# Kernel optimization log

Hardware: AMD Instinct MI355X
Metric: run time of the kernel (lower is better)

## Reference

```python
import jax, jax.numpy as jnp
import numpy as np

EMB = 768
BLOCK = 64
K = EMB // BLOCK  # 12


def setup_inputs() -> dict:
    key = jax.random.key(0)
    ks = jax.random.split(key, 8)
    n, c, d, h, E, M, P = 4, 1024, 768, 12, 32, 4, 256
    seq = jax.random.normal(ks[0], (n, c, d), dtype=jnp.float32)
    attn = jax.random.uniform(ks[1], (n, h, c, c), dtype=jnp.float32)
    attn = attn / attn.sum(-1, keepdims=True)  # attention-like rows
    mention_pos = jax.random.randint(ks[2], (n, E, M), 0, c)
    hts = jax.random.randint(ks[3], (n, P, 2), 0, E)
    W_head = jax.random.normal(ks[4], (2 * d, EMB), dtype=jnp.float32) / np.sqrt(2 * d)
    W_tail = jax.random.normal(ks[5], (2 * d, EMB), dtype=jnp.float32) / np.sqrt(2 * d)
    W_bil = jax.random.normal(ks[6], (EMB * BLOCK, 97), dtype=jnp.float32) / np.sqrt(EMB * BLOCK)
    return {
        "sequence_output": seq,
        "attention": attn,
        "mention_pos": mention_pos,
        "hts": hts,
        "W_head": W_head,
        "b_head": jnp.zeros((EMB,), jnp.float32),
        "W_tail": W_tail,
        "b_tail": jnp.zeros((EMB,), jnp.float32),
        "W_bil": W_bil,
        "b_bil": jnp.zeros((97,), jnp.float32),
    }


def reference(sequence_output, attention, mention_pos, hts,
              W_head, b_head, W_tail, b_tail, W_bil, b_bil):
    n, c, d = sequence_output.shape
    h = attention.shape[1]
    P = hts.shape[1]

    bidx = jnp.arange(n)[:, None, None]
    # gather mention token embeddings: [n, E, M, d]
    m_emb = sequence_output[bidx, mention_pos]
    # entity embedding = logsumexp over mentions (single-mention case is identical)
    ent_emb = jax.nn.logsumexp(m_emb, axis=2)                      # [n, E, d]

    # per-mention attention rows: attention[i, :, pos, :] -> [n, E, M, h, c]
    att_t = jnp.transpose(attention, (0, 2, 1, 3))                 # [n, c, h, c]
    m_att = att_t[bidx, mention_pos]                               # [n, E, M, h, c]
    ent_att = m_att.mean(axis=2)                                   # [n, E, h, c]

    pidx = jnp.arange(n)[:, None]
    hs = ent_emb[pidx, hts[..., 0]]                                # [n, P, d]
    ts = ent_emb[pidx, hts[..., 1]]
    h_att = ent_att[pidx, hts[..., 0]]                             # [n, P, h, c]
    t_att = ent_att[pidx, hts[..., 1]]

    ht_att = (h_att * t_att).mean(axis=2)                          # [n, P, c]
    ht_att = ht_att / (ht_att.sum(-1, keepdims=True) + 1e-30)
    # relation context: contract('ld,rl->rd') per doc
    rs = jnp.einsum('ncd,npc->npd', sequence_output, ht_att)       # [n, P, d]

    R = n * P
    hs2 = jnp.tanh(jnp.concatenate([hs, rs], -1).reshape(R, 2 * d) @ W_head + b_head)
    ts2 = jnp.tanh(jnp.concatenate([ts, rs], -1).reshape(R, 2 * d) @ W_tail + b_tail)

    b1 = hs2.reshape(R, K, BLOCK)
    b2 = ts2.reshape(R, K, BLOCK)
    bl = (b1[:, :, :, None] * b2[:, :, None, :]).reshape(R, EMB * BLOCK)
    logits = bl @ W_bil + b_bil                                    # [R, 97]
    return logits
```

## Files before the change

### kernel.cpp

```cpp
#include <hip/hip_runtime.h>
#include <hip/hip_bf16.h>
#include <math.h>

#define ND 4
#define CL 1024
#define DD 768
#define HH 12
#define EE 32
#define MMEN 4
#define PP 256
#define EMBD 768
#define KBL 12
#define OUTD 97
#define RTOT (ND*PP)
#define NSPLIT 24

typedef unsigned short u16;
typedef __attribute__((ext_vector_type(8))) short short8;
typedef __attribute__((ext_vector_type(8))) _Float16 half8;
typedef __attribute__((ext_vector_type(4))) float f32x4;

static __device__ inline float bf16u_to_f(unsigned v){
  union { unsigned u; float f; } c; c.u = v << 16; return c.f;
}
static __device__ inline unsigned f_to_bf16u(float f){
  union { float f; unsigned u; } c; c.f = f;
  return (c.u + 0x7fffu + ((c.u >> 16) & 1u)) >> 16;
}
static __device__ inline u16 f_to_f16u(float f){
  _Float16 h = (_Float16)f;
  union { _Float16 h; u16 u; } c; c.h = h; return c.u;
}

#define GLOAD_LDS16(gp, lp) __builtin_amdgcn_global_load_lds( \
    (const __attribute__((address_space(1))) unsigned*)(gp), \
    (__attribute__((address_space(3))) unsigned*)(lp), 16, 0, 0)

__global__ __launch_bounds__(256) void k_preproc(
    const float* __restrict__ seq, const float* __restrict__ attn,
    const int* __restrict__ mpos,
    const float* __restrict__ W_head, const float* __restrict__ W_tail,
    const float* __restrict__ W_bil,
    u16* __restrict__ ent_emb_bf, u16* __restrict__ ent_att_bf,
    u16* __restrict__ seq_t_bf, u16* __restrict__ Wh_t, u16* __restrict__ Wt_t,
    u16* __restrict__ Wt2, float* __restrict__ S)
{
  __shared__ float t[32][33];
  __shared__ __align__(16) u16 lds2[4480];
  const int bid = blockIdx.x;
  const int tid = threadIdx.x;

  if (bid < 384) {
    int idx = bid*256 + tid;
    if (idx < RTOT) S[idx] = 0.f;
    int dd = idx % DD;
    int e  = (idx / DD) % EE;
    int i  = idx / (DD*EE);
    const int* mp = mpos + (i*EE + e)*MMEN;
    float v[MMEN];
    float mx = -1e30f;
    #pragma unroll
    for (int m=0;m<MMEN;m++){
      v[m] = seq[(i*CL + mp[m])*DD + dd];
      mx = fmaxf(mx, v[m]);
    }
    float s = 0.f;
    #pragma unroll
    for (int m=0;m<MMEN;m++) s += expf(v[m]-mx);
    ent_emb_bf[idx] = (u16)f_to_bf16u(mx + logf(s));
  }
  else if (bid < 1152) {
    int idx = (bid-384)*256 + tid;
    int j8   = idx % (CL/8);
    int head = (idx / (CL/8)) % HH;
    int e    = (idx / (CL/8*HH)) % EE;
    int i    = idx / (CL/8*HH*EE);
    const int* mp = mpos + (i*EE + e)*MMEN;
    float acc[8] = {};
    #pragma unroll
    for (int m=0;m<MMEN;m++){
      const float4* p = (const float4*)(attn +
          ((size_t)(i*HH + head)*CL + mp[m])*CL + j8*8);
      float4 a = p[0], b = p[1];
      acc[0]+=a.x; acc[1]+=a.y; acc[2]+=a.z; acc[3]+=a.w;
      acc[4]+=b.x; acc[5]+=b.y; acc[6]+=b.z; acc[7]+=b.w;
    }
    unsigned o[4];
    #pragma unroll
    for (int q=0;q<4;q++){
      unsigned lo = f_to_bf16u(acc[2*q]   * (1.f/MMEN));
      unsigned hi = f_to_bf16u(acc[2*q+1] * (1.f/MMEN));
      o[q] = lo | (hi<<16);
    }
    ((uint4*)ent_att_bf)[idx] = make_uint4(o[0],o[1],o[2],o[3]);
  }
  else if (bid < 4224) {
    int l = bid - 1152;
    int bx = l % 24;
    int by = (l / 24) % 32;
    int bz = l / 768;
    const int R = CL, C = DD;
    const float* src = seq + (size_t)bz*R*C;
    u16* dst = seq_t_bf + (size_t)bz*R*C;
    int tx = tid & 31, ty = tid >> 5;
    int c0 = bx*32, r0 = by*32;
    #pragma unroll
    for (int q=0;q<4;q++)
      t[ty+8*q][tx] = src[(size_t)(r0+ty+8*q)*C + c0+tx];
    __syncthreads();
    #pragma unroll
    for (int q=0;q<4;q++)
      dst[(size_t)(c0+ty+8*q)*R + r0+tx] = (u16)f_to_bf16u(t[tx][ty+8*q]);
  }
  else if (bid < 6528) {
    int l = bid - 4224;
    int bx = l % 24;
    int by = (l / 24) % 48;
    int bz = l / 1152;
    const int R = 1536, C = DD;
    const float* src = bz ? W_tail : W_head;
    u16* dst         = bz ? Wt_t   : Wh_t;
    int tx = tid & 31, ty = tid >> 5;
    int c0 = bx*32, r0 = by*32;
    #pragma unroll
    for (int q=0;q<4;q++)
      t[ty+8*q][tx] = src[(size_t)(r0+ty+8*q)*C + c0+tx];
    __syncthreads();
    #pragma unroll
    for (int q=0;q<4;q++)
      dst[(size_t)(c0+ty+8*q)*R + r0+tx] = (u16)f_to_bf16u(t[tx][ty+8*q]);
  }
  else {
    int cc = bid - 6528;
    for (int u=tid; u<4480; u+=256) lds2[u] = 0;
    __syncthreads();
    for (int u=tid; u<112*32; u+=256){
      int kk = u / 112, n = u % 112;
      if (n < OUTD)
        lds2[n*40 + kk] = f_to_f16u(W_bil[(size_t)(cc*32 + kk)*OUTD + n]);
    }
    __syncthreads();
    uint4* dst = (uint4*)(Wt2 + (size_t)cc*4480);
    const uint4* src = (const uint4*)lds2;
    for (int v=tid; v<560; v+=256) dst[v] = src[v];
  }
}

__global__ __launch_bounds__(256) void k_ht_att(const u16* __restrict__ ent_att_bf,
    const int* __restrict__ hts, u16* __restrict__ u_ht_bf, float* __restrict__ S)
{
  const int j0  = blockIdx.x*64;
  const int pb  = blockIdx.y*64;
  const int doc = blockIdx.z;
  const int tid = threadIdx.x;
  const int p_local = tid >> 2, quad = tid & 3;
  const int grow = doc*PP + pb + p_local;
  const int he = hts[grow*2+0], te = hts[grow*2+1];
  const u16* ha = ent_att_bf + ((size_t)(doc*EE + he)*HH)*CL;
  const u16* ta = ent_att_bf + ((size_t)(doc*EE + te)*HH)*CL;
  const int jj = j0 + quad*16;

  float acc[16] = {};
  #pragma unroll
  for (int h=0; h<HH; h++){
    const uint4* pa = (const uint4*)(ha + h*CL + jj);
    const uint4* pb4 = (const uint4*)(ta + h*CL + jj);
    uint4 a0 = pa[0], a1 = pa[1];
    uint4 b0 = pb4[0], b1 = pb4[1];
    unsigned ua[8] = {a0.x,a0.y,a0.z,a0.w,a1.x,a1.y,a1.z,a1.w};
    unsigned ub[8] = {b0.x,b0.y,b0.z,b0.w,b1.x,b1.y,b1.z,b1.w};
    #pragma unroll
    for (int q=0;q<8;q++){
      acc[2*q]   += bf16u_to_f(ua[q]&0xffffu) * bf16u_to_f(ub[q]&0xffffu);
      acc[2*q+1] += bf16u_to_f(ua[q]>>16)     * bf16u_to_f(ub[q]>>16);
    }
  }
  float sum = 0.f;
  unsigned o[8];
  #pragma unroll
  for (int q=0;q<8;q++){
    float v0 = acc[2*q]   * (1.f/HH);
    float v1 = acc[2*q+1] * (1.f/HH);
    sum += v0 + v1;
    o[q] = f_to_bf16u(v0) | (f_to_bf16u(v1)<<16);
  }
  uint4* dst = (uint4*)(u_ht_bf + (size_t)grow*CL + jj);
  dst[0] = make_uint4(o[0],o[1],o[2],o[3]);
  dst[1] = make_uint4(o[4],o[5],o[6],o[7]);
  sum += __shfl_xor(sum, 1, 64);
  sum += __shfl_xor(sum, 2, 64);
  if (quad == 0) atomicAdd(&S[grow], sum);
}

__global__ __launch_bounds__(256) void k_gemm_rs_mfma(
    const u16* __restrict__ u_ht_bf, const u16* __restrict__ seq_t_bf,
    const float* __restrict__ S, u16* __restrict__ rs_bf)
{
  const int rt = blockIdx.x, ct = blockIdx.y, doc = blockIdx.z;
  const u16* A  = u_ht_bf + (size_t)doc*PP*CL;
  const u16* Bt = seq_t_bf + (size_t)doc*DD*CL;
  const int row0 = rt*64, col0 = ct*64;
  __shared__ __align__(16) u16 As[64*64];
  __shared__ __align__(16) u16 Bs[64*64];
  const int tid = threadIdx.x, lane = tid & 63, wave = tid >> 6;
  const int m = lane & 15, j8 = lane >> 4;
  const int srow8 = lane >> 3, sc8 = lane & 7;
  f32x4 acc[4];
  #pragma unroll
  for (int b=0;b<4;b++) acc[b] = (f32x4){0.f,0.f,0.f,0.f};

  for (int k0 = 0; k0 < CL; k0 += 64){
    __syncthreads();
    #pragma unroll
    for (int ii=0; ii<2; ii++){
      int row = ii*32 + wave*8 + srow8;
      int gc = sc8 ^ (row & 7);
      const u16* gpA = A + (size_t)(row0+row)*CL + k0 + gc*8;
      GLOAD_LDS16(gpA, &As[(ii*32 + wave*8)*64]);
      const u16* gpB = Bt + (size_t)(col0+row)*CL + k0 + gc*8;
      GLOAD_LDS16(gpB, &Bs[(ii*32 + wave*8)*64]);
    }
    __syncthreads();
    #pragma unroll
    for (int h=0; h<2; h++){
      short8 af, bf[4];
      {
        int r = wave*16 + m;
        int c = (h*4 + j8) ^ (r & 7);
        af = *(const short8*)&As[r*64 + c*8];
      }
      #pragma unroll
      for (int nt=0; nt<4; nt++){
        int n = nt*16 + m;
        int c = (h*4 + j8) ^ (n & 7);
        bf[nt] = *(const short8*)&Bs[n*64 + c*8];
      }
      #pragma unroll
      for (int nt=0; nt<4; nt++)
        acc[nt] = __builtin_amdgcn_mfma_f32_16x16x32_bf16(af, bf[nt], acc[nt], 0,0,0);
    }
  }

  float sc[4];
  #pragma unroll
  for (int reg=0; reg<4; reg++){
    int rowg = doc*PP + row0 + wave*16 + j8*4 + reg;
    sc[reg] = 1.f / (S[rowg] + 1e-30f);
  }
  #pragma unroll
  for (int nt=0; nt<4; nt++){
    int colg = col0 + nt*16 + m;
    #pragma unroll
    for (int reg=0; reg<4; reg++){
      int rowg = doc*PP + row0 + wave*16 + j8*4 + reg;
      rs_bf[(size_t)rowg*DD + colg] = (u16)f_to_bf16u(acc[nt][reg] * sc[reg]);
    }
  }
}

__global__ __launch_bounds__(256) void k_gemm_ht_mfma(
    const u16* __restrict__ ent_emb_bf, const u16* __restrict__ rs_bf,
    const int* __restrict__ hts,
    const u16* __restrict__ Wht, const u16* __restrict__ Wtt,
    const float* __restrict__ b_head, const float* __restrict__ b_tail,
    u16* __restrict__ hs2h, u16* __restrict__ ts2h)
{
  const int rt = blockIdx.x, ct = blockIdx.y, z = blockIdx.z;
  const u16* Bt   = z ? Wtt : Wht;
  const float* bias = z ? b_tail : b_head;
  u16* C          = z ? ts2h : hs2h;
  const int row0 = rt*128, col0 = ct*64;
  __shared__ __align__(16) u16 As[128*64];
  __shared__ __align__(16) u16 Bs[64*64];
  const int tid = threadIdx.x, lane = tid & 63, wave = tid >> 6;
  const int m = lane & 15, j8 = lane >> 4;
  const int srow8 = lane >> 3, sc8 = lane & 7;

  const u16* gEnt[4]; const u16* gRs[4]; int gcA[4];
  #pragma unroll
  for (int ii=0; ii<4; ii++){
    int row  = ii*32 + wave*8 + srow8;
    int grow = row0 + row;
    int ent  = hts[grow*2 + z];
    gEnt[ii] = ent_emb_bf + ((size_t)((grow>>8)*EE + ent))*DD;
    gRs[ii]  = rs_bf + (size_t)grow*DD;
    gcA[ii]  = (sc8 ^ (row & 7)) * 8;
  }

  f32x4 acc[2][4];
  #pragma unroll
  for (int a=0;a<2;a++)
    #pragma unroll
    for (int b=0;b<4;b++) acc[a][b] = (f32x4){0.f,0.f,0.f,0.f};

  for (int k0 = 0; k0 < 1536; k0 += 64){
    __syncthreads();
    #pragma unroll
    for (int ii=0; ii<4; ii++){
      const u16* gp = (k0 < DD) ? (gEnt[ii] + k0 + gcA[ii])
                                : (gRs[ii] + (k0-DD) + gcA[ii]);
      GLOAD_LDS16(gp, &As[(ii*32 + wave*8)*64]);
    }
    #pragma unroll
    for (int ii=0; ii<2; ii++){
      int row = ii*32 + wave*8 + srow8;
      int gc = sc8 ^ (row & 7);
      const u16* gp = Bt + (size_t)(col0+row)*1536 + k0 + gc*8;
      GLOAD_LDS16(gp, &Bs[(ii*32 + wave*8)*64]);
    }
    __syncthreads();
    #pragma unroll
    for (int h=0; h<2; h++){
      short8 af[2], bf[4];
      #pragma unroll
      for (int mf=0; mf<2; mf++){
        int r = wave*32 + mf*16 + m;
        int c = (h*4 + j8) ^ (r & 7);
        af[mf] = *(const short8*)&As[r*64 + c*8];
      }
      #pragma unroll
      for (int nt=0; nt<4; nt++){
        int n = nt*16 + m;
        int c = (h*4 + j8) ^ (n & 7);
        bf[nt] = *(const short8*)&Bs[n*64 + c*8];
      }
      #pragma unroll
      for (int mf=0; mf<2; mf++)
        #pragma unroll
        for (int nt=0; nt<4; nt++)
          acc[mf][nt] = __builtin_amdgcn_mfma_f32_16x16x32_bf16(af[mf], bf[nt], acc[mf][nt], 0,0,0);
    }
  }

  #pragma unroll
  for (int mf=0; mf<2; mf++){
    #pragma unroll
    for (int nt=0; nt<4; nt++){
      int colg = col0 + nt*16 + m;
      float bv = bias[colg];
      #pragma unroll
      for (int reg=0; reg<4; reg++){
        int rowg = row0 + wave*32 + mf*16 + j8*4 + reg;
        C[(size_t)rowg*DD + colg] = f_to_f16u(tanhf(acc[mf][nt][reg] + bv));
      }
    }
  }
}

__global__ __launch_bounds__(256) void k_bilinear(
    const u16* __restrict__ hs2h, const u16* __restrict__ ts2h,
    const u16* __restrict__ Wt2, float* __restrict__ pbuf)
{
  const int rt = blockIdx.x;
  const int sp = blockIdx.y;
  const int kb = sp >> 1;
  const int i0 = (sp & 1) * 32;
  const int row0 = rt * 128;

  __shared__ __align__(16) u16 b1s[128][40];
  __shared__ __align__(16) u16 b2s[128][72];
  __shared__ __align__(16) u16 Ws[4][4480];

  const int tid = threadIdx.x;
  const int lane = tid & 63, wave = tid >> 6;
  const int m = lane & 15, j8 = lane >> 4;

  #pragma unroll
  for (int q=0;q<2;q++){
    int u = tid + q*256;
    int r = u >> 2, seg = u & 3;
    uint4 v = *(const uint4*)&hs2h[(size_t)(row0+r)*EMBD + kb*64 + i0 + seg*8];
    *(uint4*)&b1s[r][seg*8] = v;
  }
  #pragma unroll
  for (int q=0;q<4;q++){
    int u = tid + q*256;
    int r = u >> 3, seg = u & 7;
    uint4 v = *(const uint4*)&ts2h[(size_t)(row0+r)*EMBD + kb*64 + seg*8];
    *(uint4*)&b2s[r][seg*8] = v;
  }

  const uint4* gsrc = (const uint4*)(Wt2 + (size_t)(sp*64)*4480);
  uint4* ws4 = (uint4*)Ws;
  uint4 pf0,pf1,pf2,pf3,pf4,pf5,pf6,pf7,pf8;
  pf0 = gsrc[tid];        pf1 = gsrc[tid+256];  pf2 = gsrc[tid+512];
  pf3 = gsrc[tid+768];    pf4 = gsrc[tid+1024]; pf5 = gsrc[tid+1280];
  pf6 = gsrc[tid+1536];   pf7 = gsrc[tid+1792];
  if (tid < 192) pf8 = gsrc[tid+2048];

  f32x4 acc[2][7];
  #pragma unroll
  for (int f=0;f<2;f++)
    #pragma unroll
    for (int nt=0;nt<7;nt++) acc[f][nt] = (f32x4){0.f,0.f,0.f,0.f};

  for (int s=0; s<16; s++){
    __syncthreads();
    ws4[tid]      = pf0; ws4[tid+256]  = pf1; ws4[tid+512]  = pf2;
    ws4[tid+768]  = pf3; ws4[tid+1024] = pf4; ws4[tid+1280] = pf5;
    ws4[tid+1536] = pf6; ws4[tid+1792] = pf7;
    if (tid < 192) ws4[tid+2048] = pf8;
    if (s+1 < 16){
      size_t b = (size_t)(s+1)*2240;
      pf0 = gsrc[b+tid];      pf1 = gsrc[b+tid+256];  pf2 = gsrc[b+tid+512];
      pf3 = gsrc[b+tid+768];  pf4 = gsrc[b+tid+1024]; pf5 = gsrc[b+tid+1280];
      pf6 = gsrc[b+tid+1536]; pf7 = gsrc[b+tid+1792];
      if (tid < 192) pf8 = gsrc[b+tid+2048];
    }
    __syncthreads();

    #pragma unroll
    for (int qq=0; qq<4; qq++){
      const int c = s*4 + qq;
      const int i_rel = c >> 1;
      const int j0 = (c & 1) * 32;

      half8 bfr[7];
      #pragma unroll
      for (int nt=0;nt<7;nt++)
        bfr[nt] = *(const half8*)&Ws[qq][(nt*16 + m)*40 + j8*8];

      #pragma unroll
      for (int f=0;f<2;f++){
        int r = wave*32 + f*16 + m;
        _Float16 sv1 = *(const _Float16*)&b1s[r][i_rel];
        half8 sv = {sv1,sv1,sv1,sv1,sv1,sv1,sv1,sv1};
        half8 b2v = *(const half8*)&b2s[r][j0 + j8*8];
        half8 af = sv * b2v;
        #pragma unroll
        for (int nt=0;nt<7;nt++)
          acc[f][nt] = __builtin_amdgcn_mfma_f32_16x16x32_f16(af, bfr[nt], acc[f][nt], 0, 0, 0);
      }
    }
  }

  float* dst = pbuf + ((size_t)sp*RTOT + row0)*112;
  #pragma unroll
  for (int f=0;f<2;f++){
    #pragma unroll
    for (int nt=0;nt<7;nt++){
      int col = nt*16 + m;
      #pragma unroll
      for (int reg=0;reg<4;reg++){
        int lrow = wave*32 + f*16 + j8*4 + reg;
        dst[(size_t)lrow*112 + col] = acc[f][nt][reg];
      }
    }
  }
}

__global__ __launch_bounds__(256) void k_reduce_logits(
    const float* __restrict__ pbuf, const float* __restrict__ b_bil,
    float* __restrict__ logits)
{
  int idx = blockIdx.x*256 + threadIdx.x;
  if (idx >= RTOT*112) return;
  int col = idx % 112, row = idx / 112;
  if (col >= OUTD) return;
  float s0 = 0.f, s1 = 0.f, s2 = 0.f, s3 = 0.f;
  const size_t stride = (size_t)RTOT*112;
  #pragma unroll
  for (int sp=0; sp<NSPLIT; sp+=4){
    s0 += pbuf[(sp+0)*stride + idx];
    s1 += pbuf[(sp+1)*stride + idx];
    s2 += pbuf[(sp+2)*stride + idx];
    s3 += pbuf[(sp+3)*stride + idx];
  }
  logits[(size_t)row*OUTD + col] = (s0+s1) + (s2+s3) + b_bil[col];
}

extern "C" void kernel_launch(void* const* d_in, const int* in_sizes, int n_in,
                              void* d_out, int out_size, void* d_ws, size_t ws_size,
                              hipStream_t stream)
{
  const float* seq    = (const float*)d_in[0];
  const float* attn   = (const float*)d_in[1];
  const int*   mpos   = (const int*)d_in[2];
  const int*   hts    = (const int*)d_in[3];
  const float* W_head = (const float*)d_in[4];
  const float* b_head = (const float*)d_in[5];
  const float* W_tail = (const float*)d_in[6];
  const float* b_tail = (const float*)d_in[7];
  const float* W_bil  = (const float*)d_in[8];
  const float* b_bil  = (const float*)d_in[9];
  float* logits = (float*)d_out;

  float* ws = (float*)d_ws;
  u16*   ent_emb_bf = (u16*)(ws + 0);
  float* S          = ws + 49152;
  u16*   rs_bf      = (u16*)(ws + 50176);
  u16*   hs2h       = (u16*)(ws + 443392);
  u16*   ts2h       = (u16*)(ws + 836608);
  u16*   Wh_t       = (u16*)(ws + 1229824);
  u16*   Wt_t       = (u16*)(ws + 1819648);
  u16*   ent_att_bf = (u16*)(ws + 2409472);
  u16*   u_ht_bf    = (u16*)(ws + 3195904);
  u16*   seq_t_bf   = (u16*)(ws + 3720192);
  u16*   Wt2        = (u16*)(ws + 5293056);
  float* pbuf       = ws + 8733696;

  k_preproc<<<8064, 256, 0, stream>>>(seq, attn, mpos, W_head, W_tail, W_bil,
      ent_emb_bf, ent_att_bf, seq_t_bf, Wh_t, Wt_t, Wt2, S);
  k_ht_att<<<dim3(16, 4, 4), 256, 0, stream>>>(ent_att_bf, hts, u_ht_bf, S);
  k_gemm_rs_mfma<<<dim3(4, 12, 4), 256, 0, stream>>>(u_ht_bf, seq_t_bf, S, rs_bf);
  k_gemm_ht_mfma<<<dim3(8, 12, 2), 256, 0, stream>>>(ent_emb_bf, rs_bf, hts,
      Wh_t, Wt_t, b_head, b_tail, hs2h, ts2h);
  k_bilinear<<<dim3(RTOT/128, NSPLIT), 256, 0, stream>>>(hs2h, ts2h, Wt2, pbuf);
  k_reduce_logits<<<(RTOT*112+255)/256, 256, 0, stream>>>(pbuf, b_bil, logits);
}
```

Measured before the change: 347.2 us.

## Double bilinear split-K and reduce partials with atomics into bias-initialized logits

Raises the bilinear split-K factor from 24 to 48, so each block handles 16 rows of the head chunk and half as many weight stages. The partial-sum buffer and the separate reduce kernel are removed. Logits are pre-filled with the bias during preprocessing, and each bilinear block atomically adds its partial results. This trades one kernel launch and the partial-buffer write/read traffic for float atomics, which make the summation order nondeterministic and could contend on the same addresses.

```diff
diff --git a/kernel.cpp b/kernel.cpp
--- a/kernel.cpp
+++ b/kernel.cpp
@@ -13,7 +13,7 @@
 #define KBL 12
 #define OUTD 97
 #define RTOT (ND*PP)
-#define NSPLIT 24
+#define NSPLIT 48
 
 typedef unsigned short u16;
 typedef __attribute__((ext_vector_type(8))) short short8;
@@ -40,10 +40,10 @@
     const float* __restrict__ seq, const float* __restrict__ attn,
     const int* __restrict__ mpos,
     const float* __restrict__ W_head, const float* __restrict__ W_tail,
-    const float* __restrict__ W_bil,
+    const float* __restrict__ W_bil, const float* __restrict__ b_bil,
     u16* __restrict__ ent_emb_bf, u16* __restrict__ ent_att_bf,
     u16* __restrict__ seq_t_bf, u16* __restrict__ Wh_t, u16* __restrict__ Wt_t,
-    u16* __restrict__ Wt2, float* __restrict__ S)
+    u16* __restrict__ Wt2, float* __restrict__ S, float* __restrict__ logits)
 {
   __shared__ float t[32][33];
   __shared__ __align__(16) u16 lds2[4480];
@@ -71,6 +71,7 @@
   }
   else if (bid < 1152) {
     int idx = (bid-384)*256 + tid;
+    if (idx < RTOT*OUTD) logits[idx] = b_bil[idx % OUTD];
     int j8   = idx % (CL/8);
     int head = (idx / (CL/8)) % HH;
     int e    = (idx / (CL/8*HH)) % EE;
@@ -349,15 +350,15 @@
 
 __global__ __launch_bounds__(256) void k_bilinear(
     const u16* __restrict__ hs2h, const u16* __restrict__ ts2h,
-    const u16* __restrict__ Wt2, float* __restrict__ pbuf)
+    const u16* __restrict__ Wt2, float* __restrict__ logits)
 {
   const int rt = blockIdx.x;
   const int sp = blockIdx.y;
-  const int kb = sp >> 1;
-  const int i0 = (sp & 1) * 32;
+  const int kb = sp >> 2;
+  const int i0 = (sp & 3) * 16;
   const int row0 = rt * 128;
 
-  __shared__ __align__(16) u16 b1s[128][40];
+  __shared__ __align__(16) u16 b1s[128][24];
   __shared__ __align__(16) u16 b2s[128][72];
   __shared__ __align__(16) u16 Ws[4][4480];
 
@@ -365,12 +366,10 @@
   const int lane = tid & 63, wave = tid >> 6;
   const int m = lane & 15, j8 = lane >> 4;
 
-  #pragma unroll
-  for (int q=0;q<2;q++){
-    int u = tid + q*256;
-    int r = u >> 2, seg = u & 3;
-    uint4 v = *(const uint4*)&hs2h[(size_t)(row0+r)*EMBD + kb*64 + i0 + seg*8];
-    *(uint4*)&b1s[r][seg*8] = v;
+  {
+    int r = tid >> 1, half = tid & 1;
+    uint4 v = *(const uint4*)&hs2h[(size_t)(row0+r)*EMBD + kb*64 + i0 + half*8];
+    *(uint4*)&b1s[r][half*8] = v;
   }
   #pragma unroll
   for (int q=0;q<4;q++){
@@ -380,7 +379,7 @@
     *(uint4*)&b2s[r][seg*8] = v;
   }
 
-  const uint4* gsrc = (const uint4*)(Wt2 + (size_t)(sp*64)*4480);
+  const uint4* gsrc = (const uint4*)(Wt2 + (size_t)(sp*32)*4480);
   uint4* ws4 = (uint4*)Ws;
   uint4 pf0,pf1,pf2,pf3,pf4,pf5,pf6,pf7,pf8;
   pf0 = gsrc[tid];        pf1 = gsrc[tid+256];  pf2 = gsrc[tid+512];
@@ -394,13 +393,13 @@
     #pragma unroll
     for (int nt=0;nt<7;nt++) acc[f][nt] = (f32x4){0.f,0.f,0.f,0.f};
 
-  for (int s=0; s<16; s++){
+  for (int s=0; s<8; s++){
     __syncthreads();
     ws4[tid]      = pf0; ws4[tid+256]  = pf1; ws4[tid+512]  = pf2;
     ws4[tid+768]  = pf3; ws4[tid+1024] = pf4; ws4[tid+1280] = pf5;
     ws4[tid+1536] = pf6; ws4[tid+1792] = pf7;
     if (tid < 192) ws4[tid+2048] = pf8;
-    if (s+1 < 16){
+    if (s+1 < 8){
       size_t b = (size_t)(s+1)*2240;
       pf0 = gsrc[b+tid];      pf1 = gsrc[b+tid+256];  pf2 = gsrc[b+tid+512];
       pf3 = gsrc[b+tid+768];  pf4 = gsrc[b+tid+1024]; pf5 = gsrc[b+tid+1280];
@@ -434,39 +433,20 @@
     }
   }
 
-  float* dst = pbuf + ((size_t)sp*RTOT + row0)*112;
   #pragma unroll
   for (int f=0;f<2;f++){
     #pragma unroll
     for (int nt=0;nt<7;nt++){
       int col = nt*16 + m;
-      #pragma unroll
-      for (int reg=0;reg<4;reg++){
-        int lrow = wave*32 + f*16 + j8*4 + reg;
-        dst[(size_t)lrow*112 + col] = acc[f][nt][reg];
-      }
-    }
-  }
-}
-
-__global__ __launch_bounds__(256) void k_reduce_logits(
-    const float* __restrict__ pbuf, const float* __restrict__ b_bil,
-    float* __restrict__ logits)
-{
-  int idx = blockIdx.x*256 + threadIdx.x;
-  if (idx >= RTOT*112) return;
-  int col = idx % 112, row = idx / 112;
-  if (col >= OUTD) return;
-  float s0 = 0.f, s1 = 0.f, s2 = 0.f, s3 = 0.f;
-  const size_t stride = (size_t)RTOT*112;
-  #pragma unroll
-  for (int sp=0; sp<NSPLIT; sp+=4){
-    s0 += pbuf[(sp+0)*stride + idx];
-    s1 += pbuf[(sp+1)*stride + idx];
-    s2 += pbuf[(sp+2)*stride + idx];
-    s3 += pbuf[(sp+3)*stride + idx];
-  }
-  logits[(size_t)row*OUTD + col] = (s0+s1) + (s2+s3) + b_bil[col];
+      if (col < OUTD){
+        #pragma unroll
+        for (int reg=0;reg<4;reg++){
+          int lrow = wave*32 + f*16 + j8*4 + reg;
+          atomicAdd(&logits[(size_t)(row0+lrow)*OUTD + col], acc[f][nt][reg]);
+        }
+      }
+    }
+  }
 }
 
 extern "C" void kernel_launch(void* const* d_in, const int* in_sizes, int n_in,
@@ -497,14 +477,12 @@
   u16*   u_ht_bf    = (u16*)(ws + 3195904);
   u16*   seq_t_bf   = (u16*)(ws + 3720192);
   u16*   Wt2        = (u16*)(ws + 5293056);
-  float* pbuf       = ws + 8733696;
 
   k_preproc<<<8064, 256, 0, stream>>>(seq, attn, mpos, W_head, W_tail, W_bil,
-      ent_emb_bf, ent_att_bf, seq_t_bf, Wh_t, Wt_t, Wt2, S);
+      b_bil, ent_emb_bf, ent_att_bf, seq_t_bf, Wh_t, Wt_t, Wt2, S, logits);
   k_ht_att<<<dim3(16, 4, 4), 256, 0, stream>>>(ent_att_bf, hts, u_ht_bf, S);
   k_gemm_rs_mfma<<<dim3(4, 12, 4), 256, 0, stream>>>(u_ht_bf, seq_t_bf, S, rs_bf);
   k_gemm_ht_mfma<<<dim3(8, 12, 2), 256, 0, stream>>>(ent_emb_bf, rs_bf, hts,
       Wh_t, Wt_t, b_head, b_tail, hs2h, ts2h);
-  k_bilinear<<<dim3(RTOT/128, NSPLIT), 256, 0, stream>>>(hs2h, ts2h, Wt2, pbuf);
-  k_reduce_logits<<<(RTOT*112+255)/256, 256, 0, stream>>>(pbuf, b_bil, logits);
-}
+  k_bilinear<<<dim3(RTOT/128, NSPLIT), 256, 0, stream>>>(hs2h, ts2h, Wt2, logits);
+}
```

Result: slower. 369.8 us (+6.5%).
